# Kernel tuning notes

Hardware: AMD Instinct MI355X
Metric: run time of the kernel (lower is better)

## Reference

```python
import jax, jax.numpy as jnp
import numpy as np

N_NODES = 325
C = 64
BATCH = 64
SEQ = 12
K = 3


def setup_inputs() -> dict:
    key = jax.random.key(0)
    k1, k2, k3 = jax.random.split(key, 3)
    x = jax.random.normal(k1, (BATCH, C, N_NODES, SEQ), dtype=jnp.float32)
    # sparse-ish binary adjacency with self loops (typical traffic graph density)
    a = (jax.random.uniform(k2, (N_NODES, N_NODES)) < 0.05).astype(jnp.float32)
    adj = jnp.maximum(a, a.T)
    adj = adj.at[jnp.arange(N_NODES), jnp.arange(N_NODES)].set(1.0)
    W = jax.random.normal(k3, (K, C, C), dtype=jnp.float32) * (1.0 / np.sqrt(C))
    b = jnp.zeros((C,), dtype=jnp.float32)
    return {"x": x, "adj": adj, "W": W, "b": b}


def reference(x, adj, W, b):
    B, c_in, N, T = x.shape
    # [B, C, N, T] -> [B*T, N, C]
    xr = jnp.transpose(x, (0, 3, 2, 1)).reshape(-1, N, c_in)
    # symmetric normalized Laplacian L = I - D^{-1/2} A D^{-1/2}
    d = adj.sum(axis=-1)
    d_inv_sqrt = jnp.where(d > 0, jax.lax.rsqrt(d), 0.0)
    norm_adj = d_inv_sqrt[:, None] * adj * d_inv_sqrt[None, :]
    L = jnp.eye(N, dtype=adj.dtype) - norm_adj
    # Chebyshev recursion, K=3
    Tx0 = xr
    Tx1 = jnp.einsum('ij,bjc->bic', L, Tx0)
    out = jnp.einsum('bnc,cd->bnd', Tx0, W[0]) + jnp.einsum('bnc,cd->bnd', Tx1, W[1])
    Tx2 = 2.0 * jnp.einsum('ij,bjc->bic', L, Tx1) - Tx0
    out = out + jnp.einsum('bnc,cd->bnd', Tx2, W[2]) + b
    # [B*T, N, C] -> [B, C, N, T]
    out = out.reshape(B, T, N, c_in)
    return jnp.transpose(out, (0, 3, 2, 1))
```

## Files before the change

### kernel.cpp

```cpp
#include <hip/hip_runtime.h>
#include <hip/hip_bf16.h>

#define NND   325
#define SEQ   12
#define NT    3900
#define KP    352
#define NC    11
#define CHUNK_SHORTS 12288
#define CHUNK_BYTES  24576
#define COLS  48
#define NROW  328
#define GROW  3936

typedef __attribute__((ext_vector_type(8))) short short8;
typedef __attribute__((ext_vector_type(4))) float floatx4;

static __device__ __forceinline__ unsigned short f2bf(float f) {
    unsigned int u = __float_as_uint(f);
    unsigned int r = (u + 0x7fffu + ((u >> 16) & 1u)) >> 16;
    return (unsigned short)r;
}

static __device__ __forceinline__ int xi(int m, int j) {
    int slot = (j >> 3) ^ ((m >> 1) & 3);
    return m * KP + slot * 8 + (j & 7);
}

__global__ void calc_dis(const float* __restrict__ adj, float* __restrict__ dis) {
    int i = blockIdx.x;
    const float* row = adj + (size_t)i * NND;
    float s = 0.f;
    for (int j = threadIdx.x; j < NND; j += 64) s += row[j];
    for (int o = 32; o; o >>= 1) s += __shfl_down(s, o);
    if (threadIdx.x == 0) dis[i] = (s > 0.f) ? rsqrtf(s) : 0.f;
}

__global__ void build_all(const float* __restrict__ adj, const float* __restrict__ dis,
                          unsigned short* __restrict__ Lg2,
                          const float* __restrict__ W, unsigned short* __restrict__ wflat) {
    int blk = blockIdx.x;
    if (blk < 528) {
        int s = blk * 256 + threadIdx.x;
        int c = s / CHUNK_SHORTS, r = s - c * CHUNK_SHORTS;
        int n = r >> 5, w = r & 31;
        int j = c * 32 + w;
        float v = 0.f;
        if (n < NND && j < NND) {
            float a = adj[(size_t)n * NND + j];
            v = ((n == j) ? 1.f : 0.f) - dis[n] * a * dis[j];
        }
        Lg2[s] = f2bf(v);
    } else {
        int idx = (blk - 528) * 256 + threadIdx.x;
        if (idx >= 64 * 192) return;
        int d = idx / 192, k = idx - d * 192;
        int kind = k >> 6, c = k & 63;
        float wv = W[kind * 4096 + c * 64 + d];
        float w;
        if (kind == 0)      w = wv - W[2 * 4096 + c * 64 + d];
        else if (kind == 1) w = wv;
        else                w = 2.f * wv;
        wflat[idx] = f2bf(w);
    }
}

__global__ __launch_bounds__(448, 4) void cheb_fused(
        const float* __restrict__ x,
        const unsigned short* __restrict__ Lg2,
        unsigned short* __restrict__ Yg,
        unsigned short* __restrict__ Zg) {
    __shared__ __align__(16) unsigned short img[COLS * KP];

    const int tid = threadIdx.x;
    int bid = blockIdx.x;
    bid = (bid & 7) * 128 + (bid >> 3);
    const int g0 = bid * 4;

    const int w  = tid >> 6;
    const int l  = tid & 63;
    const int lm = l & 15, lg = l >> 4;

    const char* lbase[3];
    #pragma unroll
    for (int i = 0; i < 3; ++i) {
        int nrow = (w * 3 + i) * 16 + lm;
        lbase[i] = (const char*)Lg2 + nrow * 64 + lg * 16;
    }

    for (int i = tid; i < 1056; i += 448) {
        int g = i / 264, r = i - g * 264;
        int jq = r / 3, tq = r - (r / 3) * 3;
        int j0 = jq * 4, t0 = tq * 4;
        float a[4][4];
        #pragma unroll
        for (int rr = 0; rr < 4; ++rr) {
            int j = j0 + rr;
            if (j < NND) {
                float4 v = *(const float4*)(x + (size_t)(g0 + g) * NT + j * SEQ + t0);
                a[rr][0] = v.x; a[rr][1] = v.y; a[rr][2] = v.z; a[rr][3] = v.w;
            } else {
                a[rr][0] = a[rr][1] = a[rr][2] = a[rr][3] = 0.f;
            }
        }
        #pragma unroll
        for (int s = 0; s < 4; ++s) {
            ushort4 o;
            o.x = f2bf(a[0][s]); o.y = f2bf(a[1][s]);
            o.z = f2bf(a[2][s]); o.w = f2bf(a[3][s]);
            *(ushort4*)&img[xi(g * SEQ + t0 + s, j0)] = o;
        }
    }
    __syncthreads();

    floatx4 acc[3][3];
    auto zero_acc = [&]() {
        #pragma unroll
        for (int a = 0; a < 3; ++a)
            #pragma unroll
            for (int b2 = 0; b2 < 3; ++b2) acc[a][b2] = (floatx4){0.f, 0.f, 0.f, 0.f};
    };

    auto gemm = [&]() {
        for (int c = 0; c < NC; ++c) {
            short8 lf[3];
            #pragma unroll
            for (int i = 0; i < 3; ++i)
                lf[i] = *(const short8*)(lbase[i] + c * CHUNK_BYTES);
            #pragma unroll
            for (int ct = 0; ct < 3; ++ct) {
                short8 df = *(const short8*)&img[xi(ct * 16 + lm, c * 32 + lg * 8)];
                #pragma unroll
                for (int i = 0; i < 3; ++i)
                    acc[i][ct] = __builtin_amdgcn_mfma_f32_16x16x32_bf16(
                        lf[i], df, acc[i][ct], 0, 0, 0);
            }
        }
    };

    auto store_acc = [&]() {
        #pragma unroll
        for (int i = 0; i < 3; ++i) {
            int n0 = (w * 3 + i) * 16 + lg * 4;
            #pragma unroll
            for (int ct = 0; ct < 3; ++ct) {
                ushort4 u;
                u.x = f2bf(acc[i][ct][0]); u.y = f2bf(acc[i][ct][1]);
                u.z = f2bf(acc[i][ct][2]); u.w = f2bf(acc[i][ct][3]);
                *(ushort4*)&img[xi(ct * 16 + lm, n0)] = u;
            }
        }
    };

    auto copy_out = [&](unsigned short* dst) {
        for (int i = tid; i < 4 * SEQ * 41; i += 448) {
            int gl = i / 492, r2 = i - gl * 492;
            int t = r2 / 41, oct = r2 - t * 41;
            int m = gl * SEQ + t;
            short8 v = *(const short8*)&img[xi(m, oct * 8)];
            *(short8*)&dst[(size_t)(g0 + gl) * GROW + t * NROW + oct * 8] = v;
        }
    };

    zero_acc();
    gemm();
    __syncthreads();
    store_acc();
    __syncthreads();
    copy_out(Yg);

    zero_acc();
    gemm();
    __syncthreads();
    store_acc();
    __syncthreads();
    copy_out(Zg);
}

__global__ __launch_bounds__(256) void mix2(
        const float* __restrict__ x,
        const unsigned short* __restrict__ Yg,
        const unsigned short* __restrict__ Zg,
        const unsigned short* __restrict__ wflat,
        const float* __restrict__ bias,
        float* __restrict__ out) {
    __shared__ __align__(16) unsigned char Bl[96 * 400];
    const int tid = threadIdx.x;
    int lin = blockIdx.x;
    lin = (lin & 7) * 328 + (lin >> 3);
    const int b = lin / 41;
    const int tile = lin - b * 41;
    const int nt0 = tile * 96;
    const int nn0 = tile * 8;

    for (int i = tid; i < 576; i += 256) {
        int kk = i / 192;
        int r2 = i - kk * 192;
        int cq = r2 / 12;
        int tc = r2 - cq * 12;
        int k0 = kk * 64 + cq * 4;
        unsigned short hv[4][8];
        if (kk == 0) {
            int nt = nt0 + tc * 8;
            #pragma unroll
            for (int r = 0; r < 4; ++r) {
                const float* sp = x + ((size_t)b * 64 + cq * 4 + r) * NT + nt;
                float4 v0 = (nt <= NT - 4) ? *(const float4*)sp : make_float4(0.f,0.f,0.f,0.f);
                float4 v1 = (nt <= NT - 8) ? *(const float4*)(sp + 4) : make_float4(0.f,0.f,0.f,0.f);
                hv[r][0] = f2bf(v0.x); hv[r][1] = f2bf(v0.y);
                hv[r][2] = f2bf(v0.z); hv[r][3] = f2bf(v0.w);
                hv[r][4] = f2bf(v1.x); hv[r][5] = f2bf(v1.y);
                hv[r][6] = f2bf(v1.z); hv[r][7] = f2bf(v1.w);
            }
        } else {
            const unsigned short* base = (kk == 1) ? Yg : Zg;
            #pragma unroll
            for (int r = 0; r < 4; ++r) {
                short8 s = *(const short8*)(base + ((size_t)b * 64 + cq * 4 + r) * GROW
                                            + tc * NROW + nn0);
                hv[r][0] = (unsigned short)s[0]; hv[r][1] = (unsigned short)s[1];
                hv[r][2] = (unsigned short)s[2]; hv[r][3] = (unsigned short)s[3];
                hv[r][4] = (unsigned short)s[4]; hv[r][5] = (unsigned short)s[5];
                hv[r][6] = (unsigned short)s[6]; hv[r][7] = (unsigned short)s[7];
            }
        }
        const int slot = k0 >> 3;
        const int half = (k0 & 4) << 1;
        #pragma unroll
        for (int jj = 0; jj < 8; ++jj) {
            int q = (kk == 0) ? (tc * 8 + jj) : (jj * 12 + tc);
            int sl = (slot & ~3) | ((slot & 3) ^ ((q >> 3) & 3));
            ushort4 o;
            o.x = hv[0][jj]; o.y = hv[1][jj]; o.z = hv[2][jj]; o.w = hv[3][jj];
            *(ushort4*)(Bl + q * 400 + sl * 16 + half) = o;
        }
    }
    __syncthreads();

    const int w = tid >> 6;
    const int l = tid & 63;
    const int lm = l & 15, lg = l >> 4;

    floatx4 acc[6];
    #pragma unroll
    for (int i = 0; i < 6; ++i) acc[i] = (floatx4){0.f, 0.f, 0.f, 0.f};

    const int arow = w * 16 + lm;
    const unsigned short* Ab = wflat + arow * 192;
    #pragma unroll
    for (int ks = 0; ks < 6; ++ks) {
        short8 a = *(const short8*)(Ab + ks * 32 + lg * 8);
        #pragma unroll
        for (int ni = 0; ni < 6; ++ni) {
            int q = ni * 16 + lm;
            short8 bb = *(const short8*)(Bl + q * 400 + (4 * ks + (lg ^ ((q >> 3) & 3))) * 16);
            acc[ni] = __builtin_amdgcn_mfma_f32_16x16x32_bf16(a, bb, acc[ni], 0, 0, 0);
        }
    }

    float br[4];
    #pragma unroll
    for (int j = 0; j < 4; ++j) br[j] = bias[w * 16 + lg * 4 + j];
    #pragma unroll
    for (int ni = 0; ni < 6; ++ni) {
        int nt = nt0 + ni * 16 + lm;
        if (nt < NT) {
            float* op = out + ((size_t)b * 64 + w * 16 + lg * 4) * NT + nt;
            #pragma unroll
            for (int j = 0; j < 4; ++j) op[(size_t)j * NT] = acc[ni][j] + br[j];
        }
    }
}

extern "C" void kernel_launch(void* const* d_in, const int* in_sizes, int n_in,
                              void* d_out, int out_size, void* d_ws, size_t ws_size,
                              hipStream_t stream) {
    const float* x   = (const float*)d_in[0];
    const float* adj = (const float*)d_in[1];
    const float* W   = (const float*)d_in[2];
    const float* b   = (const float*)d_in[3];
    float* out = (float*)d_out;

    char* ws = (char*)d_ws;
    float* dis           = (float*)(ws + 0);
    unsigned short* Lg2  = (unsigned short*)(ws + 1312);
    unsigned short* wflat= (unsigned short*)(ws + 271648);
    unsigned short* Yg   = (unsigned short*)(ws + 296320);
    unsigned short* Zg   = (unsigned short*)(ws + 32540032);

    calc_dis<<<NND, 64, 0, stream>>>(adj, dis);
    build_all<<<576, 256, 0, stream>>>(adj, dis, Lg2, W, wflat);
    cheb_fused<<<1024, 448, 0, stream>>>(x, Lg2, Yg, Zg);
    mix2<<<2624, 256, 0, stream>>>(x, Yg, Zg, wflat, b, out);
}
```

Measured before the change: 103.1 us.

## Precompute L squared and compute L·X and L²·X in one GEMM pass

Adds a small MFMA kernel that forms L² from the bf16 Laplacian and stores it alongside L in a concatenated layout. The main kernel then computes L·X and L²·X with a single pass over the staged X, using six row tiles per wave instead of two sequential dependent GEMMs. The second GEMM no longer has to wait on the first result written back to shared memory, which shortens the dependency chain and removes one LDS round trip. In exchange it adds an extra launch, doubles per-wave accumulators (register pressure at 448 threads with 4 blocks/SM bound), and changes numerics because L² is rounded to bf16 before being applied.

```diff
diff --git a/kernel.cpp b/kernel.cpp
--- a/kernel.cpp
+++ b/kernel.cpp
@@ -6,8 +6,8 @@
 #define NT    3900
 #define KP    352
 #define NC    11
-#define CHUNK_SHORTS 12288
-#define CHUNK_BYTES  24576
+#define CH2_SHORTS 22528
+#define CH2_BYTES  45056
 #define COLS  48
 #define NROW  328
 #define GROW  3936
@@ -36,22 +36,22 @@
 }
 
 __global__ void build_all(const float* __restrict__ adj, const float* __restrict__ dis,
-                          unsigned short* __restrict__ Lg2,
+                          unsigned short* __restrict__ Lcat,
                           const float* __restrict__ W, unsigned short* __restrict__ wflat) {
     int blk = blockIdx.x;
-    if (blk < 528) {
+    if (blk < 484) {
         int s = blk * 256 + threadIdx.x;
-        int c = s / CHUNK_SHORTS, r = s - c * CHUNK_SHORTS;
-        int n = r >> 5, w = r & 31;
-        int j = c * 32 + w;
+        int c = s / 11264, r = s - c * 11264;
+        int n = r >> 5, jj = r & 31;
+        int j = c * 32 + jj;
         float v = 0.f;
         if (n < NND && j < NND) {
             float a = adj[(size_t)n * NND + j];
             v = ((n == j) ? 1.f : 0.f) - dis[n] * a * dis[j];
         }
-        Lg2[s] = f2bf(v);
+        Lcat[(size_t)c * CH2_SHORTS + r] = f2bf(v);
     } else {
-        int idx = (blk - 528) * 256 + threadIdx.x;
+        int idx = (blk - 484) * 256 + threadIdx.x;
         if (idx >= 64 * 192) return;
         int d = idx / 192, k = idx - d * 192;
         int kind = k >> 6, c = k & 63;
@@ -64,9 +64,30 @@
     }
 }
 
-__global__ __launch_bounds__(448, 4) void cheb_fused(
+__global__ __launch_bounds__(256) void lsq_mfma(unsigned short* Lcat) {
+    int ww = blockIdx.x * 4 + (threadIdx.x >> 6);
+    int nt = ww / 22, mt = ww - nt * 22;
+    if (nt >= 21) return;
+    const int l = threadIdx.x & 63, lm = l & 15, lg = l >> 4;
+    const char* abase = (const char*)Lcat + (nt * 16 + lm) * 64 + lg * 16;
+    const char* bbase = (const char*)Lcat + (mt * 16 + lm) * 64 + lg * 16;
+    floatx4 acc = (floatx4){0.f, 0.f, 0.f, 0.f};
+    for (int c = 0; c < NC; ++c) {
+        short8 a = *(const short8*)(abase + c * CH2_BYTES);
+        short8 b = *(const short8*)(bbase + c * CH2_BYTES);
+        acc = __builtin_amdgcn_mfma_f32_16x16x32_bf16(a, b, acc, 0, 0, 0);
+    }
+    int m = mt * 16 + lm;
+    int cm = m >> 5, mw = m & 31;
+    unsigned short* dst = Lcat + (size_t)cm * CH2_SHORTS
+                        + (size_t)(352 + nt * 16 + lg * 4) * 32 + mw;
+    #pragma unroll
+    for (int r = 0; r < 4; ++r) dst[r * 32] = f2bf(acc[r]);
+}
+
+__global__ __launch_bounds__(448, 4) void cheb_single(
         const float* __restrict__ x,
-        const unsigned short* __restrict__ Lg2,
+        const unsigned short* __restrict__ Lcat,
         unsigned short* __restrict__ Yg,
         unsigned short* __restrict__ Zg) {
     __shared__ __align__(16) unsigned short img[COLS * KP];
@@ -80,11 +101,12 @@
     const int l  = tid & 63;
     const int lm = l & 15, lg = l >> 4;
 
-    const char* lbase[3];
-    #pragma unroll
-    for (int i = 0; i < 3; ++i) {
-        int nrow = (w * 3 + i) * 16 + lm;
-        lbase[i] = (const char*)Lg2 + nrow * 64 + lg * 16;
+    const char* lbase[6];
+    #pragma unroll
+    for (int i = 0; i < 6; ++i) {
+        int g = w * 6 + i;
+        int nrow = (g < 21) ? (g * 16 + lm) : (352 + (g - 21) * 16 + lm);
+        lbase[i] = (const char*)Lcat + nrow * 64 + lg * 16;
     }
 
     for (int i = tid; i < 1056; i += 448) {
@@ -112,35 +134,33 @@
     }
     __syncthreads();
 
-    floatx4 acc[3][3];
-    auto zero_acc = [&]() {
-        #pragma unroll
-        for (int a = 0; a < 3; ++a)
-            #pragma unroll
-            for (int b2 = 0; b2 < 3; ++b2) acc[a][b2] = (floatx4){0.f, 0.f, 0.f, 0.f};
-    };
-
-    auto gemm = [&]() {
-        for (int c = 0; c < NC; ++c) {
-            short8 lf[3];
-            #pragma unroll
-            for (int i = 0; i < 3; ++i)
-                lf[i] = *(const short8*)(lbase[i] + c * CHUNK_BYTES);
-            #pragma unroll
-            for (int ct = 0; ct < 3; ++ct) {
-                short8 df = *(const short8*)&img[xi(ct * 16 + lm, c * 32 + lg * 8)];
-                #pragma unroll
-                for (int i = 0; i < 3; ++i)
-                    acc[i][ct] = __builtin_amdgcn_mfma_f32_16x16x32_bf16(
-                        lf[i], df, acc[i][ct], 0, 0, 0);
-            }
-        }
-    };
-
-    auto store_acc = [&]() {
-        #pragma unroll
-        for (int i = 0; i < 3; ++i) {
-            int n0 = (w * 3 + i) * 16 + lg * 4;
+    floatx4 acc[6][3];
+    #pragma unroll
+    for (int a = 0; a < 6; ++a)
+        #pragma unroll
+        for (int b2 = 0; b2 < 3; ++b2) acc[a][b2] = (floatx4){0.f, 0.f, 0.f, 0.f};
+
+    for (int c = 0; c < NC; ++c) {
+        short8 lf[6];
+        #pragma unroll
+        for (int i = 0; i < 6; ++i)
+            lf[i] = *(const short8*)(lbase[i] + c * CH2_BYTES);
+        #pragma unroll
+        for (int ct = 0; ct < 3; ++ct) {
+            short8 df = *(const short8*)&img[xi(ct * 16 + lm, c * 32 + lg * 8)];
+            #pragma unroll
+            for (int i = 0; i < 6; ++i)
+                acc[i][ct] = __builtin_amdgcn_mfma_f32_16x16x32_bf16(
+                    lf[i], df, acc[i][ct], 0, 0, 0);
+        }
+    }
+    __syncthreads();
+
+    #pragma unroll
+    for (int i = 0; i < 6; ++i) {
+        int g = w * 6 + i;
+        if (g < 21) {
+            int n0 = g * 16 + lg * 4;
             #pragma unroll
             for (int ct = 0; ct < 3; ++ct) {
                 ushort4 u;
@@ -149,31 +169,43 @@
                 *(ushort4*)&img[xi(ct * 16 + lm, n0)] = u;
             }
         }
-    };
-
-    auto copy_out = [&](unsigned short* dst) {
+    }
+    __syncthreads();
+    {
         for (int i = tid; i < 4 * SEQ * 41; i += 448) {
             int gl = i / 492, r2 = i - gl * 492;
             int t = r2 / 41, oct = r2 - t * 41;
             int m = gl * SEQ + t;
             short8 v = *(const short8*)&img[xi(m, oct * 8)];
-            *(short8*)&dst[(size_t)(g0 + gl) * GROW + t * NROW + oct * 8] = v;
-        }
-    };
-
-    zero_acc();
-    gemm();
-    __syncthreads();
-    store_acc();
-    __syncthreads();
-    copy_out(Yg);
-
-    zero_acc();
-    gemm();
-    __syncthreads();
-    store_acc();
-    __syncthreads();
-    copy_out(Zg);
+            *(short8*)&Yg[(size_t)(g0 + gl) * GROW + t * NROW + oct * 8] = v;
+        }
+    }
+    __syncthreads();
+
+    #pragma unroll
+    for (int i = 0; i < 6; ++i) {
+        int g = w * 6 + i;
+        if (g >= 21) {
+            int n0 = (g - 21) * 16 + lg * 4;
+            #pragma unroll
+            for (int ct = 0; ct < 3; ++ct) {
+                ushort4 u;
+                u.x = f2bf(acc[i][ct][0]); u.y = f2bf(acc[i][ct][1]);
+                u.z = f2bf(acc[i][ct][2]); u.w = f2bf(acc[i][ct][3]);
+                *(ushort4*)&img[xi(ct * 16 + lm, n0)] = u;
+            }
+        }
+    }
+    __syncthreads();
+    {
+        for (int i = tid; i < 4 * SEQ * 41; i += 448) {
+            int gl = i / 492, r2 = i - gl * 492;
+            int t = r2 / 41, oct = r2 - t * 41;
+            int m = gl * SEQ + t;
+            short8 v = *(const short8*)&img[xi(m, oct * 8)];
+            *(short8*)&Zg[(size_t)(g0 + gl) * GROW + t * NROW + oct * 8] = v;
+        }
+    }
 }
 
 __global__ __launch_bounds__(256) void mix2(
@@ -282,13 +314,14 @@
 
     char* ws = (char*)d_ws;
     float* dis           = (float*)(ws + 0);
-    unsigned short* Lg2  = (unsigned short*)(ws + 1312);
-    unsigned short* wflat= (unsigned short*)(ws + 271648);
-    unsigned short* Yg   = (unsigned short*)(ws + 296320);
-    unsigned short* Zg   = (unsigned short*)(ws + 32540032);
+    unsigned short* Lcat = (unsigned short*)(ws + 1312);
+    unsigned short* wflat= (unsigned short*)(ws + 497024);
+    unsigned short* Yg   = (unsigned short*)(ws + 521600);
+    unsigned short* Zg   = (unsigned short*)(ws + 32765312);
 
     calc_dis<<<NND, 64, 0, stream>>>(adj, dis);
-    build_all<<<576, 256, 0, stream>>>(adj, dis, Lg2, W, wflat);
-    cheb_fused<<<1024, 448, 0, stream>>>(x, Lg2, Yg, Zg);
+    build_all<<<532, 256, 0, stream>>>(adj, dis, Lcat, W, wflat);
+    lsq_mfma<<<116, 256, 0, stream>>>(Lcat);
+    cheb_single<<<1024, 448, 0, stream>>>(x, Lcat, Yg, Zg);
     mix2<<<2624, 256, 0, stream>>>(x, Yg, Zg, wflat, b, out);
 }
```

After: 122.3 us. 1.19x slower.
